# Optimization experiments

Hardware: AMD Instinct MI355X
Metric: run time of the kernel (lower is better)

## Reference

```python
import jax, jax.numpy as jnp
import numpy as np

B, D_IN, D_OUT = 32768, 256, 256
E, H, GH, K = 8, 512, 128, 2
BALANCE_COEF = 0.01


def setup_inputs() -> dict:
    key = jax.random.key(0)
    ks = jax.random.split(key, 12)
    def w(k, shape, fan_in):
        return jax.random.normal(k, shape, jnp.float32) / np.sqrt(fan_in)
    return {
        "x":   jax.random.normal(ks[0], (B, D_IN), jnp.float32),
        # gating network params
        "gW1": w(ks[1], (D_IN, GH), D_IN), "gb1": jnp.zeros((GH,), jnp.float32),
        "gW2": w(ks[2], (GH, E), GH),      "gb2": jnp.zeros((E,), jnp.float32),
        # expert MLP params, stacked over experts: Linear->ReLU->Linear->ReLU->Linear
        "We1": w(ks[3], (E, D_IN, H), D_IN), "be1": jnp.zeros((E, H), jnp.float32),
        "We2": w(ks[4], (E, H, H), H),       "be2": jnp.zeros((E, H), jnp.float32),
        "We3": w(ks[5], (E, H, D_OUT), H),   "be3": jnp.zeros((E, D_OUT), jnp.float32),
    }


def reference(x, gW1, gb1, gW2, gb2, We1, be1, We2, be2, We3, be3):
    # Gating: MLP -> softmax -> top-k -> renormalize (eval mode: no noise, no dropout)
    logits = jnp.maximum(x @ gW1 + gb1, 0.0) @ gW2 + gb2          # [B, E]
    probs = jax.nn.softmax(logits, axis=-1)
    w, idx = jax.lax.top_k(probs, K)                              # [B, K] each
    w = w / jnp.sum(w, axis=-1, keepdims=True)
    onehot = jax.nn.one_hot(idx, E, dtype=x.dtype)                # [B, K, E]
    cw = jnp.einsum('bk,bke->be', w, onehot)                      # combine weights [B, E]

    # Expert compute + weighted combine. Loop over small fixed expert count;
    # cw is zero for unselected (token, expert) pairs, matching the masked
    # gather/scatter math of the original exactly.
    out = jnp.zeros((x.shape[0], We3.shape[-1]), x.dtype)
    for e in range(E):
        h = jnp.maximum(x @ We1[e] + be1[e], 0.0)                 # [B, H]
        h = jnp.maximum(h @ We2[e] + be2[e], 0.0)                 # [B, H]
        y = h @ We3[e] + be3[e]                                   # [B, D_OUT]
        out = out + y * cw[:, e:e + 1]

    # Aux: expert usage = sum over k slots of mean_b(indices==e)
    expert_usage = jnp.mean(jnp.sum(onehot, axis=1), axis=0)      # [E]
    balance_loss = jnp.mean((expert_usage - 1.0 / E) ** 2) * BALANCE_COEF
    return out, balance_loss, expert_usage
```

## Files before the change

kernel.cpp:

```cpp
#include <hip/hip_runtime.h>
#include <stdint.h>

#define E_ 8
#define DIN 256
#define DOUT 256
#define HID 512
#define GHID 128
#define NTOK 32768
#define NROW (NTOK * 2)
#define TABCAP 520
#define CNT_STRIDE 32

typedef float f32x4 __attribute__((ext_vector_type(4)));
typedef short bf16x8 __attribute__((ext_vector_type(8)));

__device__ __forceinline__ unsigned short f2bf(float f) {
    unsigned int u = __float_as_uint(f);
    u += 0x7FFFu + ((u >> 16) & 1u);
    return (unsigned short)(u >> 16);
}

__device__ __forceinline__ void gload_lds16(const void* g, void* l) {
    __builtin_amdgcn_global_load_lds(
        (const __attribute__((address_space(1))) unsigned int*)g,
        (__attribute__((address_space(3))) unsigned int*)l, 16, 0, 0);
}

__global__ __launch_bounds__(256) void k_transpose_bf16(
    const float* __restrict__ src, unsigned short* __restrict__ dst, int K, int N) {
    __shared__ float tile[64][65];
    int e = blockIdx.z;
    int k0 = blockIdx.x * 64, n0 = blockIdx.y * 64;
    const float* s = src + (size_t)e * K * N;
    unsigned short* d = dst + (size_t)e * N * K;
    int col = threadIdx.x & 63, ri = threadIdx.x >> 6;
#pragma unroll
    for (int it = 0; it < 16; ++it) {
        int row = it * 4 + ri;
        tile[row][col] = s[(size_t)(k0 + row) * N + n0 + col];
    }
    __syncthreads();
#pragma unroll
    for (int it = 0; it < 16; ++it) {
        int nrow = it * 4 + ri;
        d[(size_t)(n0 + nrow) * K + k0 + col] = f2bf(tile[col][nrow]);
    }
}

__global__ __launch_bounds__(256) void k_gate1(
    const float* __restrict__ x, const float* __restrict__ gW1,
    const float* __restrict__ gb1, float* __restrict__ hG) {
    __shared__ float xT[32][132];
    __shared__ float ws[32][132];
    int t = threadIdx.x;
    int tokBase = blockIdx.x * 128;
    int tx = t & 15, ty = t >> 4;
    float acc[8][8];
#pragma unroll
    for (int i = 0; i < 8; ++i)
#pragma unroll
        for (int j = 0; j < 8; ++j) acc[i][j] = 0.f;

    int stok = t >> 1;
    int skh = (t & 1) * 16;
    int wkk = t >> 3;
    int wh = (t & 7) * 16;

    for (int k0 = 0; k0 < DIN; k0 += 32) {
        const float* xr = x + (size_t)(tokBase + stok) * DIN + k0 + skh;
        float4 a0 = ((const float4*)xr)[0];
        float4 a1 = ((const float4*)xr)[1];
        float4 a2 = ((const float4*)xr)[2];
        float4 a3 = ((const float4*)xr)[3];
        xT[skh + 0][stok] = a0.x;  xT[skh + 1][stok] = a0.y;
        xT[skh + 2][stok] = a0.z;  xT[skh + 3][stok] = a0.w;
        xT[skh + 4][stok] = a1.x;  xT[skh + 5][stok] = a1.y;
        xT[skh + 6][stok] = a1.z;  xT[skh + 7][stok] = a1.w;
        xT[skh + 8][stok] = a2.x;  xT[skh + 9][stok] = a2.y;
        xT[skh + 10][stok] = a2.z; xT[skh + 11][stok] = a2.w;
        xT[skh + 12][stok] = a3.x; xT[skh + 13][stok] = a3.y;
        xT[skh + 14][stok] = a3.z; xT[skh + 15][stok] = a3.w;
        const float* wr = gW1 + (size_t)(k0 + wkk) * GHID + wh;
        *(float4*)&ws[wkk][wh + 0]  = ((const float4*)wr)[0];
        *(float4*)&ws[wkk][wh + 4]  = ((const float4*)wr)[1];
        *(float4*)&ws[wkk][wh + 8]  = ((const float4*)wr)[2];
        *(float4*)&ws[wkk][wh + 12] = ((const float4*)wr)[3];
        __syncthreads();
#pragma unroll 4
        for (int kk = 0; kk < 32; ++kk) {
            f32x4 wv0 = *(const f32x4*)&ws[kk][tx * 8];
            f32x4 wv1 = *(const f32x4*)&ws[kk][tx * 8 + 4];
            f32x4 xv0 = *(const f32x4*)&xT[kk][ty * 8];
            f32x4 xv1 = *(const f32x4*)&xT[kk][ty * 8 + 4];
            float xs[8] = {xv0.x, xv0.y, xv0.z, xv0.w, xv1.x, xv1.y, xv1.z, xv1.w};
            float wsv[8] = {wv0.x, wv0.y, wv0.z, wv0.w, wv1.x, wv1.y, wv1.z, wv1.w};
#pragma unroll
            for (int i = 0; i < 8; ++i)
#pragma unroll
                for (int j = 0; j < 8; ++j) acc[i][j] += xs[i] * wsv[j];
        }
        __syncthreads();
    }
    float4 b0 = *(const float4*)&gb1[tx * 8];
    float4 b1 = *(const float4*)&gb1[tx * 8 + 4];
#pragma unroll
    for (int i = 0; i < 8; ++i) {
        int tok = tokBase + ty * 8 + i;
        float4 o0, o1;
        o0.x = fmaxf(acc[i][0] + b0.x, 0.f); o0.y = fmaxf(acc[i][1] + b0.y, 0.f);
        o0.z = fmaxf(acc[i][2] + b0.z, 0.f); o0.w = fmaxf(acc[i][3] + b0.w, 0.f);
        o1.x = fmaxf(acc[i][4] + b1.x, 0.f); o1.y = fmaxf(acc[i][5] + b1.y, 0.f);
        o1.z = fmaxf(acc[i][6] + b1.z, 0.f); o1.w = fmaxf(acc[i][7] + b1.w, 0.f);
        float* hr = &hG[(size_t)tok * GHID + tx * 8];
        ((float4*)hr)[0] = o0;
        ((float4*)hr)[1] = o1;
    }
}

__global__ __launch_bounds__(256) void k_gate2(
    const float* __restrict__ hG, const float* __restrict__ gW2,
    const float* __restrict__ gb2, int2* __restrict__ tokE,
    float2* __restrict__ tokW, int* __restrict__ cnt) {
    __shared__ float hs[64][132];
    __shared__ float wg[GHID * E_];
    __shared__ int lcnt[E_];
    int t = threadIdx.x;
    int tokBase = blockIdx.x * 64;
#pragma unroll
    for (int i = 0; i < 4; ++i) wg[i * 256 + t] = gW2[i * 256 + t];
    if (t < E_) lcnt[t] = 0;
#pragma unroll
    for (int it = 0; it < 8; ++it) {
        int idx = it * 256 + t;
        int tok = idx >> 5, col = (idx & 31) * 4;
        float4 v = *(const float4*)&hG[(size_t)(tokBase + tok) * GHID + col];
        *(float4*)&hs[tok][col] = v;
    }
    __syncthreads();
    int tok = t >> 2, part = t & 3;
    float s[8];
#pragma unroll
    for (int e = 0; e < E_; ++e) s[e] = 0.f;
    const float* hr = &hs[tok][part * 32];
#pragma unroll 2
    for (int jq = 0; jq < 8; ++jq) {
        f32x4 hv = *(const f32x4*)&hr[jq * 4];
#pragma unroll
        for (int j = 0; j < 4; ++j) {
            float h = hv[j];
            int hidx = part * 32 + jq * 4 + j;
            f32x4 w0 = *(const f32x4*)&wg[hidx * 8];
            f32x4 w1 = *(const f32x4*)&wg[hidx * 8 + 4];
            s[0] += h * w0.x; s[1] += h * w0.y; s[2] += h * w0.z; s[3] += h * w0.w;
            s[4] += h * w1.x; s[5] += h * w1.y; s[6] += h * w1.z; s[7] += h * w1.w;
        }
    }
#pragma unroll
    for (int e = 0; e < E_; ++e) {
        s[e] += __shfl_xor(s[e], 1);
        s[e] += __shfl_xor(s[e], 2);
    }
    if (part == 0) {
        float l[8];
#pragma unroll
        for (int e = 0; e < E_; ++e) l[e] = s[e] + gb2[e];
        int i1 = 0; float b1v = l[0];
#pragma unroll
        for (int e = 1; e < E_; ++e) if (l[e] > b1v) { b1v = l[e]; i1 = e; }
        int i2 = -1; float b2v = -3.4e38f;
#pragma unroll
        for (int e = 0; e < E_; ++e) if (e != i1 && l[e] > b2v) { b2v = l[e]; i2 = e; }
        float mm = fmaxf(b1v, b2v);
        float p1 = expf(b1v - mm), p2 = expf(b2v - mm);
        float inv = 1.f / (p1 + p2);
        int gtok = tokBase + tok;
        tokE[gtok] = make_int2(i1, i2);
        tokW[gtok] = make_float2(p1 * inv, p2 * inv);
        atomicAdd(&lcnt[i1], 1);
        atomicAdd(&lcnt[i2], 1);
    }
    __syncthreads();
    if (t < E_) atomicAdd(&cnt[t * CNT_STRIDE], lcnt[t]);
}

__global__ void k_route_setup(const int* __restrict__ cnt, int* __restrict__ offs,
                              int* __restrict__ fill, int2* __restrict__ tab,
                              int* __restrict__ NT, float* __restrict__ outTail) {
    int t = threadIdx.x;
    int c[E_], nt[E_];
#pragma unroll
    for (int e = 0; e < E_; ++e) {
        c[e] = cnt[e * CNT_STRIDE];
        nt[e] = (c[e] + 127) >> 7;
    }
    if (t == 0) {
        int off = 0, ntp = 0;
        float bl = 0.f;
#pragma unroll
        for (int e = 0; e < E_; ++e) {
            offs[e] = off; off += c[e];
            fill[e] = 0;
            ntp += nt[e];
            float u = (float)c[e] / 32768.f;
            outTail[8388609 + e] = u;
            float dd = u - 0.125f;
            bl += dd * dd;
        }
        outTail[8388608] = bl * (0.01f / 8.f);
        *NT = ntp;
    }
    int maxnt = 0;
#pragma unroll
    for (int e = 0; e < E_; ++e) maxnt = max(maxnt, nt[e]);
    for (int k = t; k < maxnt; k += 64) {
        int p = 0;
#pragma unroll
        for (int e = 0; e < E_; ++e) p += min(nt[e], k);
#pragma unroll
        for (int e = 0; e < E_; ++e) {
            if (k < nt[e]) {
                tab[p] = make_int2(e, k);
                ++p;
            }
        }
    }
}

__global__ __launch_bounds__(256) void k_gather(
    const float* __restrict__ x, const int2* __restrict__ tokE,
    const float2* __restrict__ tokW, const int* __restrict__ offs,
    int* __restrict__ fill, int* __restrict__ rowTok, float* __restrict__ rowW,
    unsigned short* __restrict__ xg) {
    __shared__ int lc[E_], lbase[E_], lfill[E_];
    __shared__ int srow[512];
    int t = threadIdx.x;
    int tokBase = blockIdx.x * 256;
    if (t < E_) { lc[t] = 0; lfill[t] = 0; }
    __syncthreads();
    for (int s = t; s < 512; s += 256) {
        int token = tokBase + (s >> 1);
        int2 ee = tokE[token];
        int e = (s & 1) ? ee.y : ee.x;
        atomicAdd(&lc[e], 1);
    }
    __syncthreads();
    if (t < E_) lbase[t] = atomicAdd(&fill[t], lc[t]);
    __syncthreads();
    for (int s = t; s < 512; s += 256) {
        int token = tokBase + (s >> 1);
        int2 ee = tokE[token];
        float2 wv = tokW[token];
        int e; float w;
        if (s & 1) { e = ee.y; w = wv.y; } else { e = ee.x; w = wv.x; }
        int r = atomicAdd(&lfill[e], 1);
        int row = offs[e] + lbase[e] + r;
        srow[s] = row;
        rowTok[row] = token;
        rowW[row] = w;
    }
    __syncthreads();
    int wid = t >> 6, lane = t & 63;
    for (int s = wid; s < 512; s += 4) {
        int row = srow[s];
        int token = tokBase + (s >> 1);
        float4 v = ((const float4*)x)[(size_t)token * 64 + lane];
        ushort4 o;
        o.x = f2bf(v.x); o.y = f2bf(v.y); o.z = f2bf(v.z); o.w = f2bf(v.w);
        ((ushort4*)xg)[(size_t)row * 64 + lane] = o;
    }
}

template <int NCT>
__global__ __launch_bounds__(512, 4) void k_gemm(
    const unsigned short* __restrict__ A, const unsigned short* __restrict__ BT,
    const float* __restrict__ bias, const int* __restrict__ offs,
    const int* __restrict__ cnt, const int2* __restrict__ tab,
    const int* __restrict__ NT, int N, int K, int mode,
    unsigned short* __restrict__ Hout, float* __restrict__ outF,
    const int* __restrict__ rowTok, const float* __restrict__ rowW) {
    __shared__ __align__(16) unsigned short As[2][128 * 32];
    __shared__ __align__(16) unsigned short Bs[2][128 * 32];

    unsigned flat = blockIdx.x + (unsigned)NCT * blockIdx.y;
    unsigned xcd = flat % 8u;
    unsigned q = flat / 8u;
    unsigned ct = q % (unsigned)NCT;
    unsigned tIdx = (q / (unsigned)NCT) * 8u + xcd;

    if (tIdx >= (unsigned)*NT || tIdx >= (unsigned)TABCAP) return;
    int2 ent = tab[tIdx];
    int e = ent.x, rt = ent.y;
    int cntE = cnt[e * CNT_STRIDE];
    int rowStart = offs[e] + rt * 128;
    int valid = cntE - rt * 128;
    if (valid > 128) valid = 128;

    int t = threadIdx.x;
    int lane = t & 63, wid = t >> 6;
    int quad = lane >> 4, l15 = lane & 15;
    int waveM = wid >> 2, waveN = wid & 3;

    const unsigned short* Ablk = A + (size_t)rowStart * K;
    const unsigned short* Bblk = BT + ((size_t)e * N + (size_t)ct * 128) * K;

    int srow = t >> 2, skc = t & 3;
    int skcs = skc ^ ((srow >> 1) & 3);
    int ar = min(srow, valid - 1);
    const unsigned short* ga = Ablk + (size_t)ar * K + skcs * 8;
    const unsigned short* gb = Bblk + (size_t)srow * K + skcs * 8;
    int la = wid * 512;

    auto stage = [&](int b, int kt) {
        gload_lds16(ga + kt, &As[b][la]);
        gload_lds16(gb + kt, &Bs[b][la]);
    };

    const f32x4 zero = {0.f, 0.f, 0.f, 0.f};
    f32x4 acc[4][2];
#pragma unroll
    for (int i = 0; i < 4; ++i)
#pragma unroll
        for (int j = 0; j < 2; ++j) acc[i][j] = zero;

    int xq = quad ^ ((l15 >> 1) & 3);
    int nst = K >> 5;
    stage(0, 0);
    for (int s = 0; s < nst; ++s) {
        __syncthreads();
        if (s + 1 < nst) stage((s + 1) & 1, (s + 1) << 5);
        const unsigned short* Ab = As[s & 1];
        const unsigned short* Bb = Bs[s & 1];
        bf16x8 af[4], bf[2];
#pragma unroll
        for (int i = 0; i < 4; ++i)
            af[i] = *(const bf16x8*)&Ab[(waveM * 64 + i * 16 + l15) * 32 + xq * 8];
#pragma unroll
        for (int j = 0; j < 2; ++j)
            bf[j] = *(const bf16x8*)&Bb[(waveN * 32 + j * 16 + l15) * 32 + xq * 8];
#pragma unroll
        for (int i = 0; i < 4; ++i)
#pragma unroll
            for (int j = 0; j < 2; ++j)
                acc[i][j] = __builtin_amdgcn_mfma_f32_16x16x32_bf16(af[i], bf[j], acc[i][j], 0, 0, 0);
    }

    const float* be = bias + (size_t)e * N;
    if (mode == 0) {
#pragma unroll
        for (int i = 0; i < 4; ++i) {
#pragma unroll
            for (int r = 0; r < 4; ++r) {
                int rl = waveM * 64 + i * 16 + quad * 4 + r;
                if (rl < valid) {
                    size_t rowOff = (size_t)(rowStart + rl) * N;
#pragma unroll
                    for (int j = 0; j < 2; ++j) {
                        int col = (int)ct * 128 + waveN * 32 + j * 16 + l15;
                        float v = acc[i][j][r] + be[col];
                        Hout[rowOff + col] = f2bf(fmaxf(v, 0.f));
                    }
                }
            }
        }
    } else {
#pragma unroll
        for (int i = 0; i < 4; ++i) {
#pragma unroll
            for (int r = 0; r < 4; ++r) {
                int rl = waveM * 64 + i * 16 + quad * 4 + r;
                if (rl < valid) {
                    int row = rowStart + rl;
                    int tok = rowTok[row];
                    float w = rowW[row];
                    float* orow = outF + (size_t)tok * DOUT;
#pragma unroll
                    for (int j = 0; j < 2; ++j) {
                        int col = (int)ct * 128 + waveN * 32 + j * 16 + l15;
                        float v = (acc[i][j][r] + be[col]) * w;
                        atomicAdd(&orow[col], v);
                    }
                }
            }
        }
    }
}

extern "C" void kernel_launch(void* const* d_in, const int* in_sizes, int n_in,
                              void* d_out, int out_size, void* d_ws, size_t ws_size,
                              hipStream_t stream) {
    const float* x   = (const float*)d_in[0];
    const float* gW1 = (const float*)d_in[1];
    const float* gb1 = (const float*)d_in[2];
    const float* gW2 = (const float*)d_in[3];
    const float* gb2 = (const float*)d_in[4];
    const float* We1 = (const float*)d_in[5];
    const float* be1 = (const float*)d_in[6];
    const float* We2 = (const float*)d_in[7];
    const float* be2 = (const float*)d_in[8];
    const float* We3 = (const float*)d_in[9];
    const float* be3 = (const float*)d_in[10];
    float* out = (float*)d_out;

    uint8_t* ws = (uint8_t*)d_ws;
    size_t off = 0;
    auto alloc = [&](size_t bytes) -> void* {
        void* p = ws + off;
        off += (bytes + 255) & ~(size_t)255;
        return p;
    };
    unsigned short* WT1 = (unsigned short*)alloc((size_t)E_ * HID * DIN * 2);
    unsigned short* WT2 = (unsigned short*)alloc((size_t)E_ * HID * HID * 2);
    unsigned short* WT3 = (unsigned short*)alloc((size_t)E_ * DOUT * HID * 2);
    unsigned short* R1  = (unsigned short*)alloc((size_t)NROW * HID * 2);
    unsigned short* h1  = (unsigned short*)alloc((size_t)NROW * HID * 2);
    float*  hG     = (float*)alloc((size_t)NTOK * GHID * 4);
    int2*   tokE   = (int2*)alloc((size_t)NTOK * 8);
    float2* tokW   = (float2*)alloc((size_t)NTOK * 8);
    int*    rowTok = (int*)alloc((size_t)NROW * 4);
    float*  rowW   = (float*)alloc((size_t)NROW * 4);
    int*    cnt    = (int*)alloc(E_ * CNT_STRIDE * 4);
    int*    offs   = (int*)alloc(256);
    int*    fill   = (int*)alloc(256);
    int*    NT     = (int*)alloc(256);
    int2*   tab    = (int2*)alloc(TABCAP * 8);
    unsigned short* xg = R1;
    unsigned short* h2 = R1;

    hipMemsetAsync(d_out, 0, (size_t)out_size * 4, stream);
    hipMemsetAsync(cnt, 0, E_ * CNT_STRIDE * 4, stream);

    k_transpose_bf16<<<dim3(DIN / 64, HID / 64, E_), 256, 0, stream>>>(We1, WT1, DIN, HID);
    k_transpose_bf16<<<dim3(HID / 64, HID / 64, E_), 256, 0, stream>>>(We2, WT2, HID, HID);
    k_transpose_bf16<<<dim3(HID / 64, DOUT / 64, E_), 256, 0, stream>>>(We3, WT3, HID, DOUT);

    k_gate1<<<NTOK / 128, 256, 0, stream>>>(x, gW1, gb1, hG);
    k_gate2<<<NTOK / 64, 256, 0, stream>>>(hG, gW2, gb2, tokE, tokW, cnt);
    k_route_setup<<<1, 64, 0, stream>>>(cnt, offs, fill, tab, NT, out);
    k_gather<<<NTOK / 256, 256, 0, stream>>>(x, tokE, tokW, offs, fill, rowTok, rowW, xg);

    k_gemm<4><<<dim3(4, TABCAP), 512, 0, stream>>>(xg, WT1, be1, offs, cnt, tab, NT,
                                                   HID, DIN, 0, h1, nullptr, rowTok, rowW);
    k_gemm<4><<<dim3(4, TABCAP), 512, 0, stream>>>(h1, WT2, be2, offs, cnt, tab, NT,
                                                   HID, HID, 0, h2, nullptr, rowTok, rowW);
    k_gemm<2><<<dim3(2, TABCAP), 512, 0, stream>>>(h2, WT3, be3, offs, cnt, tab, NT,
                                                   DOUT, HID, 1, nullptr, out, rowTok, rowW);
}
```

Before: 391.1 us.

## Enlarge expert GEMM tiles to 256x256 with 64-wide K steps

The grouped expert GEMM tile grows from 128x128x32 to 256x256x64, and routing tiles are now counted in 256-row units. Each thread stages four 16-byte chunks per operand, using a new XOR swizzle over eight chunks per row, and each wave accumulates an 8x4 grid of MFMA tiles. The goal is more arithmetic per byte loaded and fewer blocks and barriers per unit of work. In exchange, LDS use rises to 128 KB per block, which allows only one block per CU. There are also far fewer blocks, and more padding waste sits in each expert's last tile.

```diff
diff --git a/kernel.cpp b/kernel.cpp
--- a/kernel.cpp
+++ b/kernel.cpp
@@ -9,6 +9,7 @@
 #define NTOK 32768
 #define NROW (NTOK * 2)
 #define TABCAP 520
+#define TAB256 264
 #define CNT_STRIDE 32
 
 typedef float f32x4 __attribute__((ext_vector_type(4)));
@@ -191,7 +192,7 @@
 #pragma unroll
     for (int e = 0; e < E_; ++e) {
         c[e] = cnt[e * CNT_STRIDE];
-        nt[e] = (c[e] + 127) >> 7;
+        nt[e] = (c[e] + 255) >> 8;
     }
     if (t == 0) {
         int off = 0, ntp = 0;
@@ -271,15 +272,15 @@
 }
 
 template <int NCT>
-__global__ __launch_bounds__(512, 4) void k_gemm(
+__global__ __launch_bounds__(512, 2) void k_gemm(
     const unsigned short* __restrict__ A, const unsigned short* __restrict__ BT,
     const float* __restrict__ bias, const int* __restrict__ offs,
     const int* __restrict__ cnt, const int2* __restrict__ tab,
     const int* __restrict__ NT, int N, int K, int mode,
     unsigned short* __restrict__ Hout, float* __restrict__ outF,
     const int* __restrict__ rowTok, const float* __restrict__ rowW) {
-    __shared__ __align__(16) unsigned short As[2][128 * 32];
-    __shared__ __align__(16) unsigned short Bs[2][128 * 32];
+    __shared__ __align__(16) unsigned short As[2][256 * 64];
+    __shared__ __align__(16) unsigned short Bs[2][256 * 64];
 
     unsigned flat = blockIdx.x + (unsigned)NCT * blockIdx.y;
     unsigned xcd = flat % 8u;
@@ -287,13 +288,13 @@
     unsigned ct = q % (unsigned)NCT;
     unsigned tIdx = (q / (unsigned)NCT) * 8u + xcd;
 
-    if (tIdx >= (unsigned)*NT || tIdx >= (unsigned)TABCAP) return;
+    if (tIdx >= (unsigned)*NT || tIdx >= (unsigned)TAB256) return;
     int2 ent = tab[tIdx];
     int e = ent.x, rt = ent.y;
     int cntE = cnt[e * CNT_STRIDE];
-    int rowStart = offs[e] + rt * 128;
-    int valid = cntE - rt * 128;
-    if (valid > 128) valid = 128;
+    int rowStart = offs[e] + rt * 256;
+    int valid = cntE - rt * 256;
+    if (valid > 256) valid = 256;
 
     int t = threadIdx.x;
     int lane = t & 63, wid = t >> 6;
@@ -301,61 +302,77 @@
     int waveM = wid >> 2, waveN = wid & 3;
 
     const unsigned short* Ablk = A + (size_t)rowStart * K;
-    const unsigned short* Bblk = BT + ((size_t)e * N + (size_t)ct * 128) * K;
-
-    int srow = t >> 2, skc = t & 3;
-    int skcs = skc ^ ((srow >> 1) & 3);
-    int ar = min(srow, valid - 1);
-    const unsigned short* ga = Ablk + (size_t)ar * K + skcs * 8;
-    const unsigned short* gb = Bblk + (size_t)srow * K + skcs * 8;
-    int la = wid * 512;
+    const unsigned short* Bblk = BT + ((size_t)e * N + (size_t)ct * 256) * K;
+
+    const unsigned short* gaP[4];
+    const unsigned short* gbP[4];
+    int laP[4];
+#pragma unroll
+    for (int it = 0; it < 4; ++it) {
+        int slot = it * 512 + t;
+        int row = slot >> 3;
+        int chk = (slot & 7) ^ (row & 7);
+        int arow = min(row, valid - 1);
+        gaP[it] = Ablk + (size_t)arow * K + chk * 8;
+        gbP[it] = Bblk + (size_t)row * K + chk * 8;
+        laP[it] = (it * 512 + wid * 64) * 8;
+    }
 
     auto stage = [&](int b, int kt) {
-        gload_lds16(ga + kt, &As[b][la]);
-        gload_lds16(gb + kt, &Bs[b][la]);
+#pragma unroll
+        for (int it = 0; it < 4; ++it) {
+            gload_lds16(gaP[it] + kt, &As[b][laP[it]]);
+            gload_lds16(gbP[it] + kt, &Bs[b][laP[it]]);
+        }
     };
 
     const f32x4 zero = {0.f, 0.f, 0.f, 0.f};
-    f32x4 acc[4][2];
-#pragma unroll
-    for (int i = 0; i < 4; ++i)
-#pragma unroll
-        for (int j = 0; j < 2; ++j) acc[i][j] = zero;
-
-    int xq = quad ^ ((l15 >> 1) & 3);
-    int nst = K >> 5;
+    f32x4 acc[8][4];
+#pragma unroll
+    for (int i = 0; i < 8; ++i)
+#pragma unroll
+        for (int j = 0; j < 4; ++j) acc[i][j] = zero;
+
+    int nst = K >> 6;
     stage(0, 0);
     for (int s = 0; s < nst; ++s) {
         __syncthreads();
-        if (s + 1 < nst) stage((s + 1) & 1, (s + 1) << 5);
+        if (s + 1 < nst) stage((s + 1) & 1, (s + 1) << 6);
         const unsigned short* Ab = As[s & 1];
         const unsigned short* Bb = Bs[s & 1];
-        bf16x8 af[4], bf[2];
-#pragma unroll
-        for (int i = 0; i < 4; ++i)
-            af[i] = *(const bf16x8*)&Ab[(waveM * 64 + i * 16 + l15) * 32 + xq * 8];
-#pragma unroll
-        for (int j = 0; j < 2; ++j)
-            bf[j] = *(const bf16x8*)&Bb[(waveN * 32 + j * 16 + l15) * 32 + xq * 8];
-#pragma unroll
-        for (int i = 0; i < 4; ++i)
-#pragma unroll
-            for (int j = 0; j < 2; ++j)
-                acc[i][j] = __builtin_amdgcn_mfma_f32_16x16x32_bf16(af[i], bf[j], acc[i][j], 0, 0, 0);
+#pragma unroll
+        for (int kk = 0; kk < 2; ++kk) {
+            bf16x8 af[8], bf[4];
+#pragma unroll
+            for (int i = 0; i < 8; ++i) {
+                int r = waveM * 128 + i * 16 + l15;
+                af[i] = *(const bf16x8*)&Ab[r * 64 + (((kk * 4 + quad) ^ (r & 7)) * 8)];
+            }
+#pragma unroll
+            for (int j = 0; j < 4; ++j) {
+                int r = waveN * 64 + j * 16 + l15;
+                bf[j] = *(const bf16x8*)&Bb[r * 64 + (((kk * 4 + quad) ^ (r & 7)) * 8)];
+            }
+#pragma unroll
+            for (int i = 0; i < 8; ++i)
+#pragma unroll
+                for (int j = 0; j < 4; ++j)
+                    acc[i][j] = __builtin_amdgcn_mfma_f32_16x16x32_bf16(af[i], bf[j], acc[i][j], 0, 0, 0);
+        }
     }
 
     const float* be = bias + (size_t)e * N;
     if (mode == 0) {
 #pragma unroll
-        for (int i = 0; i < 4; ++i) {
+        for (int i = 0; i < 8; ++i) {
 #pragma unroll
             for (int r = 0; r < 4; ++r) {
-                int rl = waveM * 64 + i * 16 + quad * 4 + r;
+                int rl = waveM * 128 + i * 16 + quad * 4 + r;
                 if (rl < valid) {
                     size_t rowOff = (size_t)(rowStart + rl) * N;
 #pragma unroll
-                    for (int j = 0; j < 2; ++j) {
-                        int col = (int)ct * 128 + waveN * 32 + j * 16 + l15;
+                    for (int j = 0; j < 4; ++j) {
+                        int col = (int)ct * 256 + waveN * 64 + j * 16 + l15;
                         float v = acc[i][j][r] + be[col];
                         Hout[rowOff + col] = f2bf(fmaxf(v, 0.f));
                     }
@@ -364,18 +381,18 @@
         }
     } else {
 #pragma unroll
-        for (int i = 0; i < 4; ++i) {
+        for (int i = 0; i < 8; ++i) {
 #pragma unroll
             for (int r = 0; r < 4; ++r) {
-                int rl = waveM * 64 + i * 16 + quad * 4 + r;
+                int rl = waveM * 128 + i * 16 + quad * 4 + r;
                 if (rl < valid) {
                     int row = rowStart + rl;
                     int tok = rowTok[row];
                     float w = rowW[row];
                     float* orow = outF + (size_t)tok * DOUT;
 #pragma unroll
-                    for (int j = 0; j < 2; ++j) {
-                        int col = (int)ct * 128 + waveN * 32 + j * 16 + l15;
+                    for (int j = 0; j < 4; ++j) {
+                        int col = (int)ct * 256 + waveN * 64 + j * 16 + l15;
                         float v = (acc[i][j][r] + be[col]) * w;
                         atomicAdd(&orow[col], v);
                     }
@@ -438,10 +455,10 @@
     k_route_setup<<<1, 64, 0, stream>>>(cnt, offs, fill, tab, NT, out);
     k_gather<<<NTOK / 256, 256, 0, stream>>>(x, tokE, tokW, offs, fill, rowTok, rowW, xg);
 
-    k_gemm<4><<<dim3(4, TABCAP), 512, 0, stream>>>(xg, WT1, be1, offs, cnt, tab, NT,
+    k_gemm<2><<<dim3(2, TAB256), 512, 0, stream>>>(xg, WT1, be1, offs, cnt, tab, NT,
                                                    HID, DIN, 0, h1, nullptr, rowTok, rowW);
-    k_gemm<4><<<dim3(4, TABCAP), 512, 0, stream>>>(h1, WT2, be2, offs, cnt, tab, NT,
+    k_gemm<2><<<dim3(2, TAB256), 512, 0, stream>>>(h1, WT2, be2, offs, cnt, tab, NT,
                                                    HID, HID, 0, h2, nullptr, rowTok, rowW);
-    k_gemm<2><<<dim3(2, TABCAP), 512, 0, stream>>>(h2, WT3, be3, offs, cnt, tab, NT,
+    k_gemm<1><<<dim3(1, TAB256), 512, 0, stream>>>(h2, WT3, be3, offs, cnt, tab, NT,
                                                    DOUT, HID, 1, nullptr, out, rowTok, rowW);
 }
```

Measured after the change: 474.9 us. 21.4% more time.
